# Optimization experiments

Measured on AMD Instinct MI355X. Metric: run time of the kernel, lower is better.

The kernel has to match this reference:

```python
import jax, jax.numpy as jnp
import numpy as np

N_VERTS = 5000
N_FACES = 10000
BATCH = 2
N_PTS = 8192
OUTER_LOOP = 4
INNER_LOOP = 50
SOLVE_SCALE = 10.0
ADAM_LR = 0.01
B1, B2, EPS = 0.9, 0.999, 1e-8


def _normalize(x, eps=1e-12):
    # torch.nn.functional.normalize(p=2, dim=-1)
    n = jnp.linalg.norm(x, axis=-1, keepdims=True)
    return x / jnp.maximum(n, eps)


def _interp_bary(tri, vw):
    # tri: [M,3,3] per-point triangle attributes, vw: [M,2] barycentric (u,v)
    bary = jnp.concatenate([vw, 1.0 - vw[:, :1] - vw[:, 1:2]], axis=-1)  # [M,3]
    return jnp.einsum('mij,mi->mj', tri, bary)


def _solve_delta_vwd(qV, fid, vw, mesh_V, mesh_F, mesh_N):
    # Newton-like correspondence solve via unrolled Adam (solve_delta_vwd).
    tri_idx = mesh_F[fid]          # [M,3]
    tri_V = mesh_V[tri_idx]        # [M,3,3]
    tri_N = mesh_N[tri_idx]        # [M,3,3]
    d0 = jnp.linalg.norm(_interp_bary(tri_V, vw) - qV, axis=-1)
    delta0 = jnp.concatenate([jnp.zeros_like(vw), d0[:, None]], axis=-1)  # [M,3]
    target = qV * SOLVE_SCALE

    def loss_fn(delta):
        w = vw + delta[:, :2]
        cV = _interp_bary(tri_V, w) * SOLVE_SCALE
        cN = _normalize(_interp_bary(tri_N, w)) * SOLVE_SCALE
        match = cV + cN * delta[:, 2:3]
        return jnp.mean((match - target) ** 2)  # F.mse_loss

    def step(carry, t):
        delta, m, v = carry
        g = jax.grad(loss_fn)(delta)
        m = B1 * m + (1.0 - B1) * g
        v = B2 * v + (1.0 - B2) * g * g
        mhat = m / (1.0 - B1 ** t)
        vhat = v / (1.0 - B2 ** t)
        delta = delta - ADAM_LR * mhat / (jnp.sqrt(vhat) + EPS)
        return (delta, m, v), None

    ts = jnp.arange(1, INNER_LOOP + 1, dtype=qV.dtype)
    zeros = jnp.zeros_like(delta0)
    (delta, _, _), _ = jax.lax.scan(step, (delta0, zeros, zeros), ts)
    return delta


def _forward(verts, mesh_V, mesh_N, mesh_F):
    b, n, _ = verts.shape
    # init_corres_spt: KNN (K=1) of query points against triangle centers
    centers = mesh_V[mesh_F].mean(axis=1)  # [F,3]
    d2 = ((verts ** 2).sum(-1)[..., None]
          + (centers ** 2).sum(-1)[None, None, :]
          - 2.0 * jnp.einsum('bnd,fd->bnf', verts, centers))  # [b,n,F]
    fidx = jnp.argmin(d2, axis=-1)                             # [b,n]
    fid = fidx.reshape(-1)
    qV = verts.reshape(-1, 3)
    vw = jnp.full((b * n, 2), 1.0 / 3.0, dtype=verts.dtype)
    # update_corres_spt (method='uvd'): outer triwalk loop.
    # triwalk is an external CPU mesh-walker; we use the module's documented
    # fallback when triwalk is None: vw <- vw + delta (face index unchanged).
    for _ in range(OUTER_LOOP):
        delta = _solve_delta_vwd(qV, fid, vw, mesh_V, mesh_F, mesh_N)
        vw = vw + delta[:, :2]
    outlier_mask = jnp.zeros((b, n), dtype=bool)  # max_dist = inf
    return fidx, vw.reshape(b, n, 2), outlier_mask


def setup_inputs() -> dict:
    key = jax.random.key(0)
    k1, k2, k3, k4 = jax.random.split(key, 4)
    mesh_V = jax.random.normal(k1, (N_VERTS, 3), dtype=jnp.float32)
    mesh_F = jax.random.randint(k2, (N_FACES, 3), 0, N_VERTS)
    mesh_N = _normalize(jax.random.normal(k3, (N_VERTS, 3), dtype=jnp.float32))
    verts = jax.random.normal(k4, (BATCH, N_PTS, 3), dtype=jnp.float32)
    return {"verts": verts, "mesh_V": mesh_V, "mesh_N": mesh_N, "mesh_F": mesh_F}


def reference(verts, mesh_V, mesh_N, mesh_F):
    return _forward(verts, mesh_V, mesh_N, mesh_F)
```

## Files before the change

kernel.cpp:

```cpp
#include <hip/hip_runtime.h>
#include <math.h>
#include <stdint.h>

constexpr int kVerts = 5000;
constexpr int kFaces = 10000;
constexpr int kPts   = 16384;
constexpr int kOuter = 4;
constexpr int kInner = 50;

#define SCALE 10.0f

#define KNN_WAVES 16
#define KNN_SEG   8
constexpr int kEighth      = kFaces / KNN_SEG;
constexpr int kPairsE      = kEighth / 2;
constexpr int kPtsPerLane  = 4;
constexpr int kPtsPerBlock = 64 * kPtsPerLane;
constexpr int kPtGroups    = kPts / kPtsPerBlock;

typedef float v2f __attribute__((ext_vector_type(2)));

struct BiasTabP { float rb[kInner + 2][2]; };
constexpr BiasTabP make_tabp() {
    BiasTabP t{};
    float b1 = 1.0f, b2 = 1.0f;
    for (int i = 0; i < kInner; ++i) {
        b1 *= 0.9f; b2 *= 0.999f;
        t.rb[i][0] = 1.0f / (1.0f - b1);
        t.rb[i][1] = 1.0f / (1.0f - b2);
    }
    t.rb[kInner][0]     = t.rb[kInner - 1][0];
    t.rb[kInner][1]     = t.rb[kInner - 1][1];
    t.rb[kInner + 1][0] = t.rb[kInner - 1][0];
    t.rb[kInner + 1][1] = t.rb[kInner - 1][1];
    return t;
}
constexpr BiasTabP kTabP = make_tabp();

__global__ __launch_bounds__(256)
void centers_kernel(const float* __restrict__ mesh_V,
                    const int*   __restrict__ mesh_F,
                    float*       __restrict__ soa)
{
    const int f = blockIdx.x * 256 + threadIdx.x;
    if (f >= kFaces) return;
    const int i0 = mesh_F[f * 3 + 0];
    const int i1 = mesh_F[f * 3 + 1];
    const int i2 = mesh_F[f * 3 + 2];
    const float cx = __fdiv_rn(__fadd_rn(__fadd_rn(mesh_V[i0*3+0], mesh_V[i1*3+0]), mesh_V[i2*3+0]), 3.0f);
    const float cy = __fdiv_rn(__fadd_rn(__fadd_rn(mesh_V[i0*3+1], mesh_V[i1*3+1]), mesh_V[i2*3+1]), 3.0f);
    const float cz = __fdiv_rn(__fadd_rn(__fadd_rn(mesh_V[i0*3+2], mesh_V[i1*3+2]), mesh_V[i2*3+2]), 3.0f);
    const float cc = __fadd_rn(__fadd_rn(__fmul_rn(cx, cx), __fmul_rn(cy, cy)),
                               __fmul_rn(cz, cz));
    soa[0 * kFaces + f] = cx;
    soa[1 * kFaces + f] = cy;
    soa[2 * kFaces + f] = cz;
    soa[3 * kFaces + f] = cc;
}

__global__ __launch_bounds__(1024, 8)
void knn_kernel(const float* __restrict__ verts,
                const float* __restrict__ soa,
                float*       __restrict__ ws_d2,
                int*         __restrict__ ws_f)
{
    __shared__ float4 s_A[kPairsE];
    __shared__ float4 s_B[kPairsE];
    __shared__ float  s_best [KNN_WAVES][kPtsPerBlock];
    __shared__ int    s_bestf[KNN_WAVES][kPtsPerBlock];

    const int tid  = threadIdx.x;
    const int lane = tid & 63;
    const int wv   = __builtin_amdgcn_readfirstlane(tid >> 6);
    const int pg   = blockIdx.x >> 3;
    const int fq   = blockIdx.x & 7;
    const int qbeg = fq * kEighth;

    for (int p = tid; p < kPairsE; p += 1024) {
        const v2f cx2 = *reinterpret_cast<const v2f*>(soa + 0 * kFaces + qbeg + 2 * p);
        const v2f cy2 = *reinterpret_cast<const v2f*>(soa + 1 * kFaces + qbeg + 2 * p);
        const v2f cz2 = *reinterpret_cast<const v2f*>(soa + 2 * kFaces + qbeg + 2 * p);
        const v2f cc2 = *reinterpret_cast<const v2f*>(soa + 3 * kFaces + qbeg + 2 * p);
        s_A[p] = make_float4(cx2.x, cx2.y, cy2.x, cy2.y);
        s_B[p] = make_float4(cz2.x, cz2.y, cc2.x, cc2.y);
    }

    v2f ndx[kPtsPerLane], ndy[kPtsPerLane], ndz[kPtsPerLane];
#pragma unroll
    for (int k = 0; k < kPtsPerLane; ++k) {
        const int p = pg * kPtsPerBlock + k * 64 + lane;
        const float qx = verts[p * 3 + 0];
        const float qy = verts[p * 3 + 1];
        const float qz = verts[p * 3 + 2];
        const float nx = -__fmul_rn(2.0f, qx);
        const float ny = -__fmul_rn(2.0f, qy);
        const float nz = -__fmul_rn(2.0f, qz);
        ndx[k] = (v2f){nx, nx};  asm("" : "+v"(ndx[k]));
        ndy[k] = (v2f){ny, ny};  asm("" : "+v"(ndy[k]));
        ndz[k] = (v2f){nz, nz};  asm("" : "+v"(ndz[k]));
    }

    float bd0[kPtsPerLane], bd1[kPtsPerLane];
    int   bf0[kPtsPerLane], bf1[kPtsPerLane];
#pragma unroll
    for (int k = 0; k < kPtsPerLane; ++k) {
        bd0[k] = INFINITY;   bd1[k] = INFINITY;
        bf0[k] = 0x7fffffff; bf1[k] = 0x7fffffff;
    }

    __syncthreads();

    const int pbeg = (wv * kPairsE) / KNN_WAVES;
    const int pend = ((wv + 1) * kPairsE) / KNN_WAVES;

#pragma unroll 2
    for (int f = pbeg; f < pend; ++f) {
        const float4 ab = s_A[f];
        const float4 zb = s_B[f];
        const v2f cx2 = (v2f){ab.x, ab.y};
        const v2f cy2 = (v2f){ab.z, ab.w};
        const v2f cz2 = (v2f){zb.x, zb.y};
        const v2f cc2 = (v2f){zb.z, zb.w};
        const int gf  = qbeg + 2 * f;
#pragma unroll
        for (int k = 0; k < kPtsPerLane; ++k) {
#pragma clang fp contract(off)
            const v2f m0   = ndx[k] * cx2;
            const v2f m1   = ndy[k] * cy2;
            const v2f m2   = ndz[k] * cz2;
            const v2f s01  = m0 + m1;
            const v2f dotn = s01 + m2;
            const v2f sv   = cc2 + dotn;
            if (sv.x < bd0[k]) { bd0[k] = sv.x; bf0[k] = gf; }
            if (sv.y < bd1[k]) { bd1[k] = sv.y; bf1[k] = gf + 1; }
        }
    }

#pragma unroll
    for (int k = 0; k < kPtsPerLane; ++k) {
        if (bd1[k] < bd0[k] || (bd1[k] == bd0[k] && bf1[k] < bf0[k])) {
            bd0[k] = bd1[k]; bf0[k] = bf1[k];
        }
        s_best [wv][k * 64 + lane] = bd0[k];
        s_bestf[wv][k * 64 + lane] = bf0[k];
    }
    __syncthreads();

    if (tid < kPtsPerBlock) {
        float best  = s_best [0][tid];
        int   bestf = s_bestf[0][tid];
#pragma unroll
        for (int w = 1; w < KNN_WAVES; ++w) {
            const float ob = s_best [w][tid];
            const int   of = s_bestf[w][tid];
            if (ob < best || (ob == best && of < bestf)) { best = ob; bestf = of; }
        }
        const int p = pg * kPtsPerBlock + tid;
        ws_d2[fq * kPts + p] = best;
        ws_f [fq * kPts + p] = bestf;
    }
}

template<int K>
__device__ __forceinline__ float qbcast(float v) {
    return __int_as_float(__builtin_amdgcn_update_dpp(
        0, __float_as_int(v), K * 0x55 , 0xF, 0xF, true));
}

__global__ __launch_bounds__(256)
void solve_kernel(const float* __restrict__ verts,
                  const float* __restrict__ mesh_V,
                  const float* __restrict__ mesh_N,
                  const int*   __restrict__ mesh_F,
                  const float* __restrict__ ws_d2,
                  const int*   __restrict__ ws_f,
                  float*       __restrict__ out)
{
    const int t  = blockIdx.x * 256 + threadIdx.x;
    const int p  = t >> 2;
    const int ch = t & 3;
    const bool isV = (ch == 1);
    const bool isD = (ch >= 2);

    float bdm = ws_d2[p];
    int   f   = ws_f[p];
#pragma unroll
    for (int q = 1; q < KNN_SEG; ++q) {
        const float d  = ws_d2[q * kPts + p];
        const int   ff = ws_f [q * kPts + p];
        if (d < bdm) { bdm = d; f = ff; }
    }
    if (ch == 0) out[p] = (float)f;

    const float qx = verts[p * 3 + 0];
    const float qy = verts[p * 3 + 1];
    const float qz = verts[p * 3 + 2];

    const int i0 = mesh_F[f * 3 + 0];
    const int i1 = mesh_F[f * 3 + 1];
    const int i2 = mesh_F[f * 3 + 2];

    const float V0x = mesh_V[i0*3+0], V0y = mesh_V[i0*3+1], V0z = mesh_V[i0*3+2];
    const float V1x = mesh_V[i1*3+0], V1y = mesh_V[i1*3+1], V1z = mesh_V[i1*3+2];
    const float V2x = mesh_V[i2*3+0], V2y = mesh_V[i2*3+1], V2z = mesh_V[i2*3+2];
    const float N0x = mesh_N[i0*3+0], N0y = mesh_N[i0*3+1], N0z = mesh_N[i0*3+2];
    const float N1x = mesh_N[i1*3+0], N1y = mesh_N[i1*3+1], N1z = mesh_N[i1*3+2];
    const float N2x = mesh_N[i2*3+0], N2y = mesh_N[i2*3+1], N2z = mesh_N[i2*3+2];

    const float E0x = V0x - V2x, E0y = V0y - V2y, E0z = V0z - V2z;
    const float E1x = V1x - V2x, E1y = V1y - V2y, E1z = V1z - V2z;
    const float F0x = N0x - N2x, F0y = N0y - N2y, F0z = N0z - N2z;
    const float F1x = N1x - N2x, F1y = N1y - N2y, F1z = N1z - N2z;

    const float Aux = isV ? E1x : E0x;
    const float Auy = isV ? E1y : E0y;
    const float Auz = isV ? E1z : E0z;
    const float Bx  = isD ? 0.0f : (isV ? F1x : F0x);
    const float By  = isD ? 0.0f : (isV ? F1y : F0y);
    const float Bz  = isD ? 0.0f : (isV ? F1z : F0z);

    const float tx = qx * SCALE, ty = qy * SCALE, tz = qz * SCALE;
    const float GS = 2.0f / (3.0f * 16384.0f);
    const float B1c = 0.9f,  ONE_M_B1 = 1.0f - 0.9f;
    const float B2c = 0.999f, ONE_M_B2 = 1.0f - 0.999f;

    float vwu = 1.0f / 3.0f, vwv = 1.0f / 3.0f;

#define SOLVE_STEP(RB1, RB2)                                                   \
    {                                                                          \
        const float du = qbcast<0>(dlt);                                       \
        const float dv = qbcast<1>(dlt);                                       \
        const float dd = qbcast<2>(dlt);                                       \
        const float bu = vwu + du;                                             \
        const float bv = vwv + dv;                                             \
        const float bw = (1.0f - bu) - bv;                                     \
        const float cVx = ((bu * V0x + bv * V1x) + bw * V2x) * SCALE;          \
        const float cVy = ((bu * V0y + bv * V1y) + bw * V2y) * SCALE;          \
        const float cVz = ((bu * V0z + bv * V1z) + bw * V2z) * SCALE;          \
        const float nrx = (bu * N0x + bv * N1x) + bw * N2x;                    \
        const float nry = (bu * N0y + bv * N1y) + bw * N2y;                    \
        const float nrz = (bu * N0z + bv * N1z) + bw * N2z;                    \
        const float nn  = (nrx * nrx + nry * nry) + nrz * nrz;                 \
        const float inv = __builtin_amdgcn_rsqf(nn);                           \
        const float nhx = nrx * inv, nhy = nry * inv, nhz = nrz * inv;         \
        const float cNx = nhx * SCALE, cNy = nhy * SCALE, cNz = nhz * SCALE;   \
        const float rx = (cVx + cNx * dd) - tx;                                \
        const float ry = (cVy + cNy * dd) - ty;                                \
        const float rz = (cVz + cNz * dd) - tz;                                \
        const float Ax = isD ? nhx : Aux;                                      \
        const float Ay = isD ? nhy : Auy;                                      \
        const float Az = isD ? nhz : Auz;                                      \
        const float dotA = (rx * Ax + ry * Ay) + rz * Az;                      \
        const float dotB = (rx * Bx + ry * By) + rz * Bz;                      \
        const float nhB  = (nhx * Bx + nhy * By) + nhz * Bz;                   \
        const float nr_r = qbcast<2>(dotA);                                    \
        const float g = GS * (SCALE * dotA + (dd * SCALE) * ((dotB - nr_r * nhB) * inv)); \
        mA = B1c * mA + ONE_M_B1 * g;                                          \
        vA = B2c * vA + ONE_M_B2 * (g * g);                                    \
        const float s = __builtin_amdgcn_rsqf(vA * (RB2) + 1e-16f);            \
        dlt -= 0.01f * (mA * (RB1)) * s;                                       \
    }

    for (int outer = 0; outer < kOuter; ++outer) {
        const float bw0 = (1.0f - vwu) - vwv;
        const float px = ((vwu * V0x + vwv * V1x) + bw0 * V2x);
        const float py = ((vwu * V0y + vwv * V1y) + bw0 * V2y);
        const float pz = ((vwu * V0z + vwv * V1z) + bw0 * V2z);
        const float dx = px - qx, dy = py - qy, dz = pz - qz;
        const float d0 = __builtin_amdgcn_sqrtf((dx * dx + dy * dy) + dz * dz);

        float dlt = isD ? d0 : 0.0f;
        float mA  = 0.0f, vA = 0.0f;

        float rbA1 = kTabP.rb[0][0], rbA2 = kTabP.rb[0][1];
        float rbB1 = kTabP.rb[1][0], rbB2 = kTabP.rb[1][1];
#pragma unroll 1
        for (int it2 = 0; it2 < kInner / 2; ++it2) {
            const float n1a = kTabP.rb[2 * it2 + 2][0];
            const float n2a = kTabP.rb[2 * it2 + 2][1];
            const float n1b = kTabP.rb[2 * it2 + 3][0];
            const float n2b = kTabP.rb[2 * it2 + 3][1];
            SOLVE_STEP(rbA1, rbA2);
            SOLVE_STEP(rbB1, rbB2);
            rbA1 = n1a; rbA2 = n2a; rbB1 = n1b; rbB2 = n2b;
        }
        vwu += qbcast<0>(dlt);
        vwv += qbcast<1>(dlt);
    }
#undef SOLVE_STEP

    if (ch == 0) {
        out[kPts + 2 * p + 0] = vwu;
        out[kPts + 2 * p + 1] = vwv;
        out[3 * kPts + p]     = 0.0f;
    }
}

extern "C" void kernel_launch(void* const* d_in, const int* in_sizes, int n_in,
                              void* d_out, int out_size, void* d_ws, size_t ws_size,
                              hipStream_t stream) {
    const float* verts  = (const float*)d_in[0];
    const float* mesh_V = (const float*)d_in[1];
    const float* mesh_N = (const float*)d_in[2];
    const int*   mesh_F = (const int*)d_in[3];
    float* out = (float*)d_out;

    float* ws_soa = (float*)d_ws;
    float* ws_d2  = (float*)((char*)d_ws + 4 * kFaces * sizeof(float));
    int*   ws_f   = (int*)((char*)ws_d2 + KNN_SEG * kPts * sizeof(float));

    hipLaunchKernelGGL(centers_kernel, dim3((kFaces + 255) / 256), dim3(256), 0, stream,
                       mesh_V, mesh_F, ws_soa);
    hipLaunchKernelGGL(knn_kernel,     dim3(kPtGroups * KNN_SEG), dim3(1024), 0, stream,
                       verts, ws_soa, ws_d2, ws_f);
    hipLaunchKernelGGL(solve_kernel,   dim3(kPts * 4 / 256), dim3(256), 0, stream,
                       verts, mesh_V, mesh_N, mesh_F, ws_d2, ws_f, out);
}
```

Baseline: 124.5 us.

## Fuse face-center computation into KNN and retune points per lane and solve threads

Removes the separate centers kernel. Each KNN block now gathers triangle vertices and computes its segment's centers and squared norms directly into shared memory, which saves a launch and a global round trip at the cost of redundant per-block recomputation. KNN points per lane double from 4 to 8, the occupancy hint drops to 4, and the argmin update becomes branchless using fmin plus a select. The solve kernel now launches 8 threads per point, so half the lanes redundantly repeat the quad's work, presumably to add waves for latency hiding.

```diff
diff --git a/kernel.cpp b/kernel.cpp
--- a/kernel.cpp
+++ b/kernel.cpp
@@ -12,9 +12,9 @@
 
 #define KNN_WAVES 16
 #define KNN_SEG   8
-constexpr int kEighth      = kFaces / KNN_SEG;
-constexpr int kPairsE      = kEighth / 2;
-constexpr int kPtsPerLane  = 4;
+constexpr int kSeg         = kFaces / KNN_SEG;
+constexpr int kPairsE      = kSeg / 2;
+constexpr int kPtsPerLane  = 8;
 constexpr int kPtsPerBlock = 64 * kPtsPerLane;
 constexpr int kPtGroups    = kPts / kPtsPerBlock;
 
@@ -37,30 +37,10 @@
 }
 constexpr BiasTabP kTabP = make_tabp();
 
-__global__ __launch_bounds__(256)
-void centers_kernel(const float* __restrict__ mesh_V,
-                    const int*   __restrict__ mesh_F,
-                    float*       __restrict__ soa)
-{
-    const int f = blockIdx.x * 256 + threadIdx.x;
-    if (f >= kFaces) return;
-    const int i0 = mesh_F[f * 3 + 0];
-    const int i1 = mesh_F[f * 3 + 1];
-    const int i2 = mesh_F[f * 3 + 2];
-    const float cx = __fdiv_rn(__fadd_rn(__fadd_rn(mesh_V[i0*3+0], mesh_V[i1*3+0]), mesh_V[i2*3+0]), 3.0f);
-    const float cy = __fdiv_rn(__fadd_rn(__fadd_rn(mesh_V[i0*3+1], mesh_V[i1*3+1]), mesh_V[i2*3+1]), 3.0f);
-    const float cz = __fdiv_rn(__fadd_rn(__fadd_rn(mesh_V[i0*3+2], mesh_V[i1*3+2]), mesh_V[i2*3+2]), 3.0f);
-    const float cc = __fadd_rn(__fadd_rn(__fmul_rn(cx, cx), __fmul_rn(cy, cy)),
-                               __fmul_rn(cz, cz));
-    soa[0 * kFaces + f] = cx;
-    soa[1 * kFaces + f] = cy;
-    soa[2 * kFaces + f] = cz;
-    soa[3 * kFaces + f] = cc;
-}
-
-__global__ __launch_bounds__(1024, 8)
+__global__ __launch_bounds__(1024, 4)
 void knn_kernel(const float* __restrict__ verts,
-                const float* __restrict__ soa,
+                const float* __restrict__ mesh_V,
+                const int*   __restrict__ mesh_F,
                 float*       __restrict__ ws_d2,
                 int*         __restrict__ ws_f)
 {
@@ -74,15 +54,27 @@
     const int wv   = __builtin_amdgcn_readfirstlane(tid >> 6);
     const int pg   = blockIdx.x >> 3;
     const int fq   = blockIdx.x & 7;
-    const int qbeg = fq * kEighth;
-
-    for (int p = tid; p < kPairsE; p += 1024) {
-        const v2f cx2 = *reinterpret_cast<const v2f*>(soa + 0 * kFaces + qbeg + 2 * p);
-        const v2f cy2 = *reinterpret_cast<const v2f*>(soa + 1 * kFaces + qbeg + 2 * p);
-        const v2f cz2 = *reinterpret_cast<const v2f*>(soa + 2 * kFaces + qbeg + 2 * p);
-        const v2f cc2 = *reinterpret_cast<const v2f*>(soa + 3 * kFaces + qbeg + 2 * p);
-        s_A[p] = make_float4(cx2.x, cx2.y, cy2.x, cy2.y);
-        s_B[p] = make_float4(cz2.x, cz2.y, cc2.x, cc2.y);
+    const int qbeg = fq * kSeg;
+
+    {
+        float* s_Af = (float*)s_A;
+        float* s_Bf = (float*)s_B;
+        for (int i = tid; i < kSeg; i += 1024) {
+            const int f  = qbeg + i;
+            const int i0 = mesh_F[f * 3 + 0];
+            const int i1 = mesh_F[f * 3 + 1];
+            const int i2 = mesh_F[f * 3 + 2];
+            const float cx = __fdiv_rn(__fadd_rn(__fadd_rn(mesh_V[i0*3+0], mesh_V[i1*3+0]), mesh_V[i2*3+0]), 3.0f);
+            const float cy = __fdiv_rn(__fadd_rn(__fadd_rn(mesh_V[i0*3+1], mesh_V[i1*3+1]), mesh_V[i2*3+1]), 3.0f);
+            const float cz = __fdiv_rn(__fadd_rn(__fadd_rn(mesh_V[i0*3+2], mesh_V[i1*3+2]), mesh_V[i2*3+2]), 3.0f);
+            const float cc = __fadd_rn(__fadd_rn(__fmul_rn(cx, cx), __fmul_rn(cy, cy)),
+                                       __fmul_rn(cz, cz));
+            const int p = i >> 1, h = i & 1;
+            s_Af[4 * p + 0 + h] = cx;
+            s_Af[4 * p + 2 + h] = cy;
+            s_Bf[4 * p + 0 + h] = cz;
+            s_Bf[4 * p + 2 + h] = cc;
+        }
     }
 
     v2f ndx[kPtsPerLane], ndy[kPtsPerLane], ndz[kPtsPerLane];
@@ -122,6 +114,7 @@
         const v2f cz2 = (v2f){zb.x, zb.y};
         const v2f cc2 = (v2f){zb.z, zb.w};
         const int gf  = qbeg + 2 * f;
+        const int gf1 = gf + 1;
 #pragma unroll
         for (int k = 0; k < kPtsPerLane; ++k) {
 #pragma clang fp contract(off)
@@ -131,8 +124,10 @@
             const v2f s01  = m0 + m1;
             const v2f dotn = s01 + m2;
             const v2f sv   = cc2 + dotn;
-            if (sv.x < bd0[k]) { bd0[k] = sv.x; bf0[k] = gf; }
-            if (sv.y < bd1[k]) { bd1[k] = sv.y; bf1[k] = gf + 1; }
+            bf0[k] = (sv.x < bd0[k]) ? gf  : bf0[k];
+            bd0[k] = __builtin_fminf(sv.x, bd0[k]);
+            bf1[k] = (sv.y < bd1[k]) ? gf1 : bf1[k];
+            bd1[k] = __builtin_fminf(sv.y, bd1[k]);
         }
     }
 
@@ -176,9 +171,10 @@
                   const int*   __restrict__ ws_f,
                   float*       __restrict__ out)
 {
-    const int t  = blockIdx.x * 256 + threadIdx.x;
-    const int p  = t >> 2;
-    const int ch = t & 3;
+    const int t   = blockIdx.x * 256 + threadIdx.x;
+    const int p   = t >> 3;
+    const int sub = t & 7;
+    const int ch  = sub & 3;
     const bool isV = (ch == 1);
     const bool isD = (ch >= 2);
 
@@ -190,7 +186,7 @@
         const int   ff = ws_f [q * kPts + p];
         if (d < bdm) { bdm = d; f = ff; }
     }
-    if (ch == 0) out[p] = (float)f;
+    if (sub == 0) out[p] = (float)f;
 
     const float qx = verts[p * 3 + 0];
     const float qy = verts[p * 3 + 1];
@@ -289,7 +285,7 @@
     }
 #undef SOLVE_STEP
 
-    if (ch == 0) {
+    if (sub == 0) {
         out[kPts + 2 * p + 0] = vwu;
         out[kPts + 2 * p + 1] = vwv;
         out[3 * kPts + p]     = 0.0f;
@@ -305,14 +301,11 @@
     const int*   mesh_F = (const int*)d_in[3];
     float* out = (float*)d_out;
 
-    float* ws_soa = (float*)d_ws;
-    float* ws_d2  = (float*)((char*)d_ws + 4 * kFaces * sizeof(float));
-    int*   ws_f   = (int*)((char*)ws_d2 + KNN_SEG * kPts * sizeof(float));
-
-    hipLaunchKernelGGL(centers_kernel, dim3((kFaces + 255) / 256), dim3(256), 0, stream,
-                       mesh_V, mesh_F, ws_soa);
-    hipLaunchKernelGGL(knn_kernel,     dim3(kPtGroups * KNN_SEG), dim3(1024), 0, stream,
-                       verts, ws_soa, ws_d2, ws_f);
-    hipLaunchKernelGGL(solve_kernel,   dim3(kPts * 4 / 256), dim3(256), 0, stream,
+    float* ws_d2 = (float*)d_ws;
+    int*   ws_f  = (int*)((char*)ws_d2 + KNN_SEG * kPts * sizeof(float));
+
+    hipLaunchKernelGGL(knn_kernel,   dim3(kPtGroups * KNN_SEG), dim3(1024), 0, stream,
+                       verts, mesh_V, mesh_F, ws_d2, ws_f);
+    hipLaunchKernelGGL(solve_kernel, dim3(kPts * 8 / 256), dim3(256), 0, stream,
                        verts, mesh_V, mesh_N, mesh_F, ws_d2, ws_f, out);
 }
```

New measurement: 145.4 us. 16.8% more time.

## Use FMA chains and eight points per lane in KNN inner loop

Applied to the files above, without the earlier changes.

The KNN kernel now processes eight query points per lane instead of four, so each face pair loaded from shared memory is reused across more points and the grid has half as many point groups. The distance evaluation changes from contract-off packed multiplies and adds to a scalar FMA chain, with branchless fmin/select argmin updates and a software-prefetched shared-memory load. Launch bounds are relaxed to allow more registers. FMA rounding differs from the reference's separate multiply and add, which may change which face wins on near-ties, and fewer blocks lower occupancy.

```diff
diff --git a/kernel.cpp b/kernel.cpp
--- a/kernel.cpp
+++ b/kernel.cpp
@@ -12,9 +12,9 @@
 
 #define KNN_WAVES 16
 #define KNN_SEG   8
-constexpr int kEighth      = kFaces / KNN_SEG;
-constexpr int kPairsE      = kEighth / 2;
-constexpr int kPtsPerLane  = 4;
+constexpr int kSeg         = kFaces / KNN_SEG;
+constexpr int kPairsE      = kSeg / 2;
+constexpr int kPtsPerLane  = 8;
 constexpr int kPtsPerBlock = 64 * kPtsPerLane;
 constexpr int kPtGroups    = kPts / kPtsPerBlock;
 
@@ -58,7 +58,7 @@
     soa[3 * kFaces + f] = cc;
 }
 
-__global__ __launch_bounds__(1024, 8)
+__global__ __launch_bounds__(1024, 4)
 void knn_kernel(const float* __restrict__ verts,
                 const float* __restrict__ soa,
                 float*       __restrict__ ws_d2,
@@ -74,7 +74,7 @@
     const int wv   = __builtin_amdgcn_readfirstlane(tid >> 6);
     const int pg   = blockIdx.x >> 3;
     const int fq   = blockIdx.x & 7;
-    const int qbeg = fq * kEighth;
+    const int qbeg = fq * kSeg;
 
     for (int p = tid; p < kPairsE; p += 1024) {
         const v2f cx2 = *reinterpret_cast<const v2f*>(soa + 0 * kFaces + qbeg + 2 * p);
@@ -85,19 +85,16 @@
         s_B[p] = make_float4(cz2.x, cz2.y, cc2.x, cc2.y);
     }
 
-    v2f ndx[kPtsPerLane], ndy[kPtsPerLane], ndz[kPtsPerLane];
+    float ndx[kPtsPerLane], ndy[kPtsPerLane], ndz[kPtsPerLane];
 #pragma unroll
     for (int k = 0; k < kPtsPerLane; ++k) {
         const int p = pg * kPtsPerBlock + k * 64 + lane;
         const float qx = verts[p * 3 + 0];
         const float qy = verts[p * 3 + 1];
         const float qz = verts[p * 3 + 2];
-        const float nx = -__fmul_rn(2.0f, qx);
-        const float ny = -__fmul_rn(2.0f, qy);
-        const float nz = -__fmul_rn(2.0f, qz);
-        ndx[k] = (v2f){nx, nx};  asm("" : "+v"(ndx[k]));
-        ndy[k] = (v2f){ny, ny};  asm("" : "+v"(ndy[k]));
-        ndz[k] = (v2f){nz, nz};  asm("" : "+v"(ndz[k]));
+        ndx[k] = -__fmul_rn(2.0f, qx);  asm("" : "+v"(ndx[k]));
+        ndy[k] = -__fmul_rn(2.0f, qy);  asm("" : "+v"(ndy[k]));
+        ndz[k] = -__fmul_rn(2.0f, qz);  asm("" : "+v"(ndz[k]));
     }
 
     float bd0[kPtsPerLane], bd1[kPtsPerLane];
@@ -113,28 +110,37 @@
     const int pbeg = (wv * kPairsE) / KNN_WAVES;
     const int pend = ((wv + 1) * kPairsE) / KNN_WAVES;
 
-#pragma unroll 2
-    for (int f = pbeg; f < pend; ++f) {
-        const float4 ab = s_A[f];
-        const float4 zb = s_B[f];
-        const v2f cx2 = (v2f){ab.x, ab.y};
-        const v2f cy2 = (v2f){ab.z, ab.w};
-        const v2f cz2 = (v2f){zb.x, zb.y};
-        const v2f cc2 = (v2f){zb.z, zb.w};
-        const int gf  = qbeg + 2 * f;
-#pragma unroll
-        for (int k = 0; k < kPtsPerLane; ++k) {
-#pragma clang fp contract(off)
-            const v2f m0   = ndx[k] * cx2;
-            const v2f m1   = ndy[k] * cy2;
-            const v2f m2   = ndz[k] * cz2;
-            const v2f s01  = m0 + m1;
-            const v2f dotn = s01 + m2;
-            const v2f sv   = cc2 + dotn;
-            if (sv.x < bd0[k]) { bd0[k] = sv.x; bf0[k] = gf; }
-            if (sv.y < bd1[k]) { bd1[k] = sv.y; bf1[k] = gf + 1; }
-        }
-    }
+#define KNN_PAIR_EVALS(AB, ZB, GF)                                            \
+    {                                                                         \
+        const int gf_  = (GF);                                                \
+        const int gf1_ = gf_ + 1;                                             \
+        _Pragma("unroll")                                                     \
+        for (int k = 0; k < kPtsPerLane; ++k) {                               \
+            const float s0 = __builtin_fmaf(ndx[k], (AB).x,                   \
+                             __builtin_fmaf(ndy[k], (AB).z,                   \
+                             __builtin_fmaf(ndz[k], (ZB).x, (ZB).z)));        \
+            const float s1 = __builtin_fmaf(ndx[k], (AB).y,                   \
+                             __builtin_fmaf(ndy[k], (AB).w,                   \
+                             __builtin_fmaf(ndz[k], (ZB).y, (ZB).w)));        \
+            bf0[k] = (s0 < bd0[k]) ? gf_  : bf0[k];                           \
+            bd0[k] = __builtin_fminf(s0, bd0[k]);                             \
+            bf1[k] = (s1 < bd1[k]) ? gf1_ : bf1[k];                           \
+            bd1[k] = __builtin_fminf(s1, bd1[k]);                             \
+        }                                                                     \
+    }
+
+    int fp = pbeg;
+    float4 a = s_A[fp];
+    float4 b = s_B[fp];
+#pragma unroll 1
+    for (; fp < pend - 1; ++fp) {
+        const float4 an = s_A[fp + 1];
+        const float4 bn = s_B[fp + 1];
+        KNN_PAIR_EVALS(a, b, qbeg + 2 * fp);
+        a = an; b = bn;
+    }
+    KNN_PAIR_EVALS(a, b, qbeg + 2 * fp);
+#undef KNN_PAIR_EVALS
 
 #pragma unroll
     for (int k = 0; k < kPtsPerLane; ++k) {
```

Result: no change. 125.5 us (+0.8%).
